# Kernel optimization log

Measured on AMD Instinct MI355X. Metric: run time of the kernel, lower is better.

Reference implementation:

```python
import jax, jax.numpy as jnp
import numpy as np

N_NODES = 100_000
E_OFF = 1_500_000
LATENT = 64
MP_STEPS = 3


def setup_inputs() -> dict:
    key = jax.random.key(0)
    ks = jax.random.split(key, 12)
    # lower-triangular graph: all self-loops + random off-diagonal edges with row >= col
    r = jax.random.randint(ks[0], (E_OFF,), 0, N_NODES)
    c = jax.random.randint(ks[1], (E_OFF,), 0, N_NODES)
    diag = jnp.arange(N_NODES)
    edge_row = jnp.concatenate([jnp.maximum(r, c), diag]).astype(jnp.int64)
    edge_col = jnp.concatenate([jnp.minimum(r, c), diag]).astype(jnp.int64)
    E = E_OFF + N_NODES
    # positive weights (gcn_norm takes deg^{-1/2} of weighted degree)
    edge_attr = jax.random.uniform(ks[2], (E,), jnp.float32) + 0.05
    x = jax.random.normal(ks[3], (N_NODES, 1), jnp.float32)
    L = LATENT
    def lin(k, fi, fo):
        return jax.random.normal(k, (fi, fo), jnp.float32) / np.sqrt(fi)
    return {
        "x": x,
        "edge_attr": edge_attr,
        "w_enc": lin(ks[4], 1, L), "b_enc": jnp.zeros((L,), jnp.float32),
        "conv1_w": jax.random.normal(ks[5], (MP_STEPS, L, L), jnp.float32) / np.sqrt(L),
        "conv1_b": jnp.zeros((MP_STEPS, L), jnp.float32),
        "conv2_w": jax.random.normal(ks[6], (MP_STEPS, L, L), jnp.float32) / np.sqrt(L),
        "conv2_b": jnp.zeros((MP_STEPS, L), jnp.float32),
        "dec_w1": lin(ks[7], 2 * L, L), "dec_b1": jnp.zeros((L,), jnp.float32),
        "dec_w2": lin(ks[8], L, 1), "dec_b2": jnp.zeros((1,), jnp.float32),
        "edge_row": edge_row,
        "edge_col": edge_col,
    }


def reference(x, edge_attr, w_enc, b_enc, conv1_w, conv1_b, conv2_w, conv2_b,
              dec_w1, dec_b1, dec_w2, dec_b2, edge_row, edge_col):
    N = x.shape[0]
    # GCN normalization (graph already contains all self-loops, so PyG's
    # add_remaining_self_loops is a no-op and keeps existing loop weights)
    deg = jax.ops.segment_sum(edge_attr, edge_col, num_segments=N)
    dinv = jnp.where(deg > 0, jax.lax.rsqrt(jnp.maximum(deg, 1e-30)), 0.0)
    norm = dinv[edge_row] * edge_attr * dinv[edge_col]  # [E]
    cnt = jnp.maximum(
        jax.ops.segment_sum(jnp.ones_like(edge_attr), edge_col, num_segments=N), 1.0
    )[:, None]  # mean aggregation denominator

    def gcn(h, W, b):
        m = (h @ W)[edge_row] * norm[:, None]           # [E, F] messages
        agg = jax.ops.segment_sum(m, edge_col, num_segments=N) / cnt
        return agg + b

    # node encoder: single Linear (no activation)
    h = x @ w_enc + b_enc
    for i in range(MP_STEPS):
        h = jax.nn.relu(gcn(h, conv1_w[i], conv1_b[i]))
        h = jax.nn.relu(gcn(h, conv2_w[i], conv2_b[i]))

    # edge decoder: gather endpoints, MLP [2L -> L -> 1]
    e = jnp.concatenate([h[edge_row], h[edge_col]], axis=1)
    e = jax.nn.relu(e @ dec_w1 + dec_b1)
    e = (e @ dec_w2 + dec_b2)[:, 0]                      # [E]
    vals = jnp.where(edge_row == edge_col, jax.nn.softplus(e), e)
    return vals
```

## Files before the change

kernel.cpp:

```cpp
#include <hip/hip_runtime.h>
#include <hip/hip_fp16.h>
#include <math.h>

#define L 64
#define FIXS 65536.0f
#define WAITCNT_LGKM0 0xC07F

#define FMAMIX_LO(acc, pkh, ws) \
    asm("v_fma_mix_f32 %0, %1, %2, %0 op_sel:[0,0,0] op_sel_hi:[1,0,0]" \
        : "+v"(acc) : "v"(pkh), "v"(ws))
#define FMAMIX_HI(acc, pkh, ws) \
    asm("v_fma_mix_f32 %0, %1, %2, %0 op_sel:[1,0,0] op_sel_hi:[1,0,0]" \
        : "+v"(acc) : "v"(pkh), "v"(ws))
#define PKADDRELU(d, a, b) \
    asm("v_pk_add_f16 %0, %1, %2\n\tv_pk_max_f16 %0, %0, 0" \
        : "=v"(d) : "v"(a), "v"(b))


__global__ void k_hist(const int* __restrict__ col, const float* __restrict__ attr,
                       unsigned* __restrict__ degcnt,
                       int* __restrict__ rank, int E) {
    int e = blockIdx.x * blockDim.x + threadIdx.x;
    if (e < E) {
        int c = col[e];
        unsigned fx = (unsigned)(int)rintf(attr[e] * FIXS);
        unsigned old = atomicAdd(&degcnt[c], (1u << 24) | fx);
        rank[e] = (int)(old >> 24);
    }
}

__global__ void k_dinv(const unsigned* __restrict__ degcnt,
                       float* __restrict__ dinv, int* __restrict__ cntI,
                       float* __restrict__ rcnt, int N) {
    int n = blockIdx.x * blockDim.x + threadIdx.x;
    if (n < N) {
        unsigned p = degcnt[n];
        unsigned cnt = p >> 24;
        float d = (float)(p & 0xFFFFFFu) * (1.0f / FIXS);
        dinv[n] = (d > 0.f) ? (1.0f / sqrtf(fmaxf(d, 1e-30f))) : 0.f;
        cntI[n] = (int)cnt;
        unsigned c = cnt ? cnt : 1u;
        rcnt[n] = 1.0f / (float)c;
    }
}


__global__ __launch_bounds__(256) void k_scan_a(const int* __restrict__ cntI,
                                                int* __restrict__ blockSums, int N) {
    __shared__ int red[4];
    int b = blockIdx.x, t = threadIdx.x;
    int base = b * 1024 + t * 4;
    int s = 0;
    #pragma unroll
    for (int i = 0; i < 4; ++i) { int idx = base + i; if (idx < N) s += cntI[idx]; }
    #pragma unroll
    for (int off = 32; off > 0; off >>= 1) s += __shfl_down(s, off);
    if ((t & 63) == 0) red[t >> 6] = s;
    __syncthreads();
    if (t == 0) blockSums[b] = red[0] + red[1] + red[2] + red[3];
}

__global__ __launch_bounds__(1024) void k_scan_b(int* __restrict__ blockSums, int B,
                                                 int* __restrict__ ptr, int N) {
    __shared__ int sh[1024];
    int t = threadIdx.x;
    sh[t] = (t < B) ? blockSums[t] : 0;
    __syncthreads();
    for (int off = 1; off < 1024; off <<= 1) {
        int v = (t >= off) ? sh[t - off] : 0;
        __syncthreads();
        sh[t] += v;
        __syncthreads();
    }
    if (t < B) blockSums[t] = (t == 0) ? 0 : sh[t - 1];
    if (t == B - 1) ptr[N] = sh[t];
}

__global__ __launch_bounds__(256) void k_scan_c(const int* __restrict__ cntI,
                                                const int* __restrict__ blockSums,
                                                int* __restrict__ ptr, int N) {
    __shared__ int th[256];
    int b = blockIdx.x, t = threadIdx.x;
    int base = b * 1024 + t * 4;
    int v[4]; int s = 0;
    #pragma unroll
    for (int i = 0; i < 4; ++i) {
        int idx = base + i;
        v[i] = (idx < N) ? cntI[idx] : 0;
        s += v[i];
    }
    th[t] = s;
    __syncthreads();
    for (int off = 1; off < 256; off <<= 1) {
        int x = (t >= off) ? th[t - off] : 0;
        __syncthreads();
        th[t] += x;
        __syncthreads();
    }
    int pre = ((t == 0) ? 0 : th[t - 1]) + blockSums[b];
    #pragma unroll
    for (int i = 0; i < 4; ++i) {
        int idx = base + i;
        if (idx < N) ptr[idx] = pre;
        pre += v[i];
    }
}

__global__ void k_scatter(const int* __restrict__ row, const int* __restrict__ col,
                          const float* __restrict__ attr, const float* __restrict__ dinv,
                          const int* __restrict__ colptr,
                          int* __restrict__ rank ,
                          unsigned* __restrict__ csrX, int E) {
    int e = blockIdx.x * blockDim.x + threadIdx.x;
    if (e < E) {
        int r = row[e], c = col[e];
        int pos = colptr[c] + rank[e];
        float nrm = dinv[r] * attr[e] * dinv[c];
        unsigned short nb = __half_as_ushort(__float2half(nrm));
        csrX[pos] = (unsigned)r | ((unsigned)nb << 17);
        rank[e] = pos;
    }
}


__global__ void k_encode(const float* __restrict__ x, const float* __restrict__ w_enc,
                         const float* __restrict__ b_enc, __half* __restrict__ h, int N) {
    int idx = blockIdx.x * blockDim.x + threadIdx.x;
    if (idx < N * L) {
        int n = idx >> 6, f = idx & 63;
        h[idx] = __float2half(x[n] * w_enc[f] + b_enc[f]);
    }
}


__global__ __launch_bounds__(256) void k_gcn(const uint2* __restrict__ h_in2,
        __half* __restrict__ h_out,
        const float* __restrict__ W, const float* __restrict__ bias,
        const int* __restrict__ colptr, const unsigned* __restrict__ csrX,
        const float* __restrict__ rcnt, int N) {
    __shared__ float sm[4][72];
    int lane = threadIdx.x & 63;
    int warp = threadIdx.x >> 6;
    int grp  = lane >> 4;
    int sub  = lane & 15;
    int wid  = (blockIdx.x * blockDim.x + threadIdx.x) >> 6;
    int nw   = (gridDim.x * blockDim.x) >> 6;
    float* smw = &sm[warp][0];

    float Wc[L];
    #pragma unroll
    for (int f = 0; f < L; ++f) Wc[f] = W[f * L + lane];
    float bl = bias[lane];

    int beg = 0, end = 0; unsigned mw = 0;
    if (wid < N) {
        beg = colptr[wid];
        end = colptr[wid + 1];
        if (beg + lane < end) mw = csrX[beg + lane];
    }

    for (int n = wid; n < N; n += nw) {
        int n2 = n + nw;
        int beg2 = 0, end2 = 0;
        if (n2 < N) { beg2 = colptr[n2]; end2 = colptr[n2 + 1]; }

        float sA0=0.f,sA1=0.f,sA2=0.f,sA3=0.f, sB0=0.f,sB1=0.f,sB2=0.f,sB3=0.f;
        float sC0=0.f,sC1=0.f,sC2=0.f,sC3=0.f, sD0=0.f,sD1=0.f,sD2=0.f,sD3=0.f;

        auto PROC = [&](unsigned mwv, int mm) {
            int kmax = (mm + 3) >> 2;
            int k = 0;
            for (; k + 4 <= kmax; k += 4) {
                int j0 = 4 * k + grp;
                unsigned x0 = (unsigned)__shfl((int)mwv, j0);
                unsigned x1 = (unsigned)__shfl((int)mwv, j0 + 4);
                unsigned x2 = (unsigned)__shfl((int)mwv, j0 + 8);
                unsigned x3 = (unsigned)__shfl((int)mwv, j0 + 12);
                int r0 = (int)(x0 & 0x1FFFFu), r1 = (int)(x1 & 0x1FFFFu);
                int r2 = (int)(x2 & 0x1FFFFu), r3 = (int)(x3 & 0x1FFFFu);
                float w0 = __half2float(__ushort_as_half((unsigned short)(x0 >> 17)));
                float w1 = __half2float(__ushort_as_half((unsigned short)(x1 >> 17)));
                float w2 = __half2float(__ushort_as_half((unsigned short)(x2 >> 17)));
                float w3 = __half2float(__ushort_as_half((unsigned short)(x3 >> 17)));
                uint2 q0 = h_in2[(size_t)r0 * 16 + sub];
                uint2 q1 = h_in2[(size_t)r1 * 16 + sub];
                uint2 q2 = h_in2[(size_t)r2 * 16 + sub];
                uint2 q3 = h_in2[(size_t)r3 * 16 + sub];
                FMAMIX_LO(sA0, q0.x, w0); FMAMIX_HI(sA1, q0.x, w0);
                FMAMIX_LO(sA2, q0.y, w0); FMAMIX_HI(sA3, q0.y, w0);
                FMAMIX_LO(sB0, q1.x, w1); FMAMIX_HI(sB1, q1.x, w1);
                FMAMIX_LO(sB2, q1.y, w1); FMAMIX_HI(sB3, q1.y, w1);
                FMAMIX_LO(sC0, q2.x, w2); FMAMIX_HI(sC1, q2.x, w2);
                FMAMIX_LO(sC2, q2.y, w2); FMAMIX_HI(sC3, q2.y, w2);
                FMAMIX_LO(sD0, q3.x, w3); FMAMIX_HI(sD1, q3.x, w3);
                FMAMIX_LO(sD2, q3.y, w3); FMAMIX_HI(sD3, q3.y, w3);
            }
            for (; k < kmax; ++k) {
                int j0 = 4 * k + grp;
                unsigned x0 = (unsigned)__shfl((int)mwv, j0);
                int   r0 = (int)(x0 & 0x1FFFFu);
                float w0 = __half2float(__ushort_as_half((unsigned short)(x0 >> 17)));
                uint2 q0 = h_in2[(size_t)r0 * 16 + sub];
                FMAMIX_LO(sA0, q0.x, w0); FMAMIX_HI(sA1, q0.x, w0);
                FMAMIX_LO(sA2, q0.y, w0); FMAMIX_HI(sA3, q0.y, w0);
            }
        };

        int m = end - beg; if (m > 64) m = 64;
        PROC(mw, m);
        for (int base = beg + 64; base < end; base += 64) {
            int mm = end - base; if (mm > 64) mm = 64;
            unsigned mwc = 0;
            if (lane < mm) mwc = csrX[base + lane];
            PROC(mwc, mm);
        }

        unsigned mw2 = 0;
        if (n2 < N && beg2 + lane < end2) mw2 = csrX[beg2 + lane];

        float sx = (sA0 + sB0) + (sC0 + sD0);
        float sy = (sA1 + sB1) + (sC1 + sD1);
        float sz = (sA2 + sB2) + (sC2 + sD2);
        float sw = (sA3 + sB3) + (sC3 + sD3);
        sx += __shfl_xor(sx, 16); sx += __shfl_xor(sx, 32);
        sy += __shfl_xor(sy, 16); sy += __shfl_xor(sy, 32);
        sz += __shfl_xor(sz, 16); sz += __shfl_xor(sz, 32);
        sw += __shfl_xor(sw, 16); sw += __shfl_xor(sw, 32);
        if (grp == 0) {
            smw[4 * sub + 0] = sx; smw[4 * sub + 1] = sy;
            smw[4 * sub + 2] = sz; smw[4 * sub + 3] = sw;
        }
        __builtin_amdgcn_s_waitcnt(WAITCNT_LGKM0);
        float a0 = 0.f, a1 = 0.f, a2 = 0.f, a3 = 0.f;
        const float4* smv = (const float4*)smw;
        #pragma unroll
        for (int q = 0; q < 16; ++q) {
            float4 sv = smv[q];
            a0 += sv.x * Wc[4 * q + 0];
            a1 += sv.y * Wc[4 * q + 1];
            a2 += sv.z * Wc[4 * q + 2];
            a3 += sv.w * Wc[4 * q + 3];
        }
        float o = ((a0 + a1) + (a2 + a3)) * rcnt[n] + bl;
        h_out[(size_t)n * L + lane] = __float2half(fmaxf(o, 0.f));

        beg = beg2; end = end2; mw = mw2;
    }
}


__global__ __launch_bounds__(256) void k_mv2(const __half* __restrict__ h,
        const float* __restrict__ W1, const float* __restrict__ b1,
        __half* __restrict__ U, __half* __restrict__ V, int N) {
    __shared__ float sm[4][72];
    int lane = threadIdx.x & 63;
    int warp = threadIdx.x >> 6;
    int wid  = (blockIdx.x * blockDim.x + threadIdx.x) >> 6;
    int nw   = (gridDim.x * blockDim.x) >> 6;
    float* smw = &sm[warp][0];
    float Wu[L], Wv[L];
    #pragma unroll
    for (int f = 0; f < L; ++f) Wu[f] = W1[f * L + lane];
    #pragma unroll
    for (int f = 0; f < L; ++f) Wv[f] = W1[(L + f) * L + lane];
    float bl = b1[lane];
    for (int n = wid; n < N; n += nw) {
        float hl = __half2float(h[(size_t)n * L + lane]);
        smw[lane] = hl;
        __builtin_amdgcn_s_waitcnt(WAITCNT_LGKM0);
        float a0 = 0.f, a1 = 0.f, c0 = 0.f, c1 = 0.f;
        const float4* smv = (const float4*)smw;
        #pragma unroll
        for (int q = 0; q < 16; ++q) {
            float4 sv = smv[q];
            a0 += sv.x * Wu[4 * q + 0] ; a1 += sv.y * Wu[4 * q + 1];
            a0 += sv.z * Wu[4 * q + 2] ; a1 += sv.w * Wu[4 * q + 3];
            c0 += sv.x * Wv[4 * q + 0] ; c1 += sv.y * Wv[4 * q + 1];
            c0 += sv.z * Wv[4 * q + 2] ; c1 += sv.w * Wv[4 * q + 3];
        }
        U[(size_t)n * L + lane] = __float2half((a0 + a1) + bl);
        V[(size_t)n * L + lane] = __float2half(c0 + c1);
        __builtin_amdgcn_s_waitcnt(WAITCNT_LGKM0);
    }
}


__global__ __launch_bounds__(256) void k_edge(const __half* __restrict__ U,
        const __half* __restrict__ V, const float* __restrict__ w2,
        const float* __restrict__ b2,
        const int* __restrict__ colptr, const unsigned* __restrict__ csrX,
        float* __restrict__ tmp, int N) {
    int lane = threadIdx.x & 63;
    int hf   = lane & 1;
    int wid  = (blockIdx.x * blockDim.x + threadIdx.x) >> 6;
    int nw   = (gridDim.x * blockDim.x) >> 6;
    float w2f[32];
    #pragma unroll
    for (int k = 0; k < 32; ++k) w2f[k] = w2[32 * hf + k];
    float b2v = b2[0];

    int beg = 0, end = 0; unsigned md0 = 0;
    if (wid < N) {
        beg = colptr[wid]; end = colptr[wid + 1];
        int ep = beg + (lane >> 1);
        if (ep < end) md0 = csrX[ep];
    }

    for (int n = wid; n < N; n += nw) {
        int n2 = n + nw;
        int beg2 = 0, end2 = 0;
        if (n2 < N) { beg2 = colptr[n2]; end2 = colptr[n2 + 1]; }

        const uint4* vrow = (const uint4*)(V + (size_t)n * L + 32 * hf);
        uint4 v0 = vrow[0], v1 = vrow[1], v2 = vrow[2], v3 = vrow[3];
        unsigned md = md0;
        for (int base = beg; base < end; base += 32) {
            int epos = base + (lane >> 1);
            if (epos < end) {
                int r = (int)(md & 0x1FFFFu);
                const uint4* urow = (const uint4*)(U + (size_t)r * L + 32 * hf);
                uint4 u0 = urow[0], u1 = urow[1], u2 = urow[2], u3 = urow[3];
                float p0 = 0.f, p1 = 0.f, p2 = 0.f, p3 = 0.f;
                #define DOT2X(uw, vw, B, pa, pb) { unsigned t_; \
                    PKADDRELU(t_, (uw), (vw)); \
                    FMAMIX_LO(pa, t_, w2f[B]); FMAMIX_HI(pb, t_, w2f[(B) + 1]); }
                DOT2X(u0.x, v0.x,  0, p0, p1) DOT2X(u0.y, v0.y,  2, p2, p3)
                DOT2X(u0.z, v0.z,  4, p0, p1) DOT2X(u0.w, v0.w,  6, p2, p3)
                DOT2X(u1.x, v1.x,  8, p0, p1) DOT2X(u1.y, v1.y, 10, p2, p3)
                DOT2X(u1.z, v1.z, 12, p0, p1) DOT2X(u1.w, v1.w, 14, p2, p3)
                DOT2X(u2.x, v2.x, 16, p0, p1) DOT2X(u2.y, v2.y, 18, p2, p3)
                DOT2X(u2.z, v2.z, 20, p0, p1) DOT2X(u2.w, v2.w, 22, p2, p3)
                DOT2X(u3.x, v3.x, 24, p0, p1) DOT2X(u3.y, v3.y, 26, p2, p3)
                DOT2X(u3.z, v3.z, 28, p0, p1) DOT2X(u3.w, v3.w, 30, p2, p3)
                #undef DOT2X
                float p = (p0 + p2) + (p1 + p3);
                p += __shfl_xor(p, 1);
                if (hf == 0) {
                    float val = p + b2v;
                    if (r == n) val = fmaxf(val, 0.f) + log1pf(expf(-fabsf(val)));
                    tmp[epos] = val;
                }
            }
            if (base + 32 < end) {
                int ep2 = base + 32 + (lane >> 1);
                md = (ep2 < end) ? csrX[ep2] : 0;
            }
        }

        unsigned mdn = 0;
        if (n2 < N) {
            int ep = beg2 + (lane >> 1);
            if (ep < end2) mdn = csrX[ep];
        }
        beg = beg2; end = end2; md0 = mdn;
    }
}


__global__ void k_perm(const int* __restrict__ epos, const float* __restrict__ tmp,
                       float* __restrict__ out, int E) {
    int e = blockIdx.x * blockDim.x + threadIdx.x;
    if (e < E) out[e] = tmp[epos[e]];
}


extern "C" void kernel_launch(void* const* d_in, const int* in_sizes, int n_in,
                              void* d_out, int out_size, void* d_ws, size_t ws_size,
                              hipStream_t stream) {
    const float* x     = (const float*)d_in[0];
    const float* attr  = (const float*)d_in[1];
    const float* w_enc = (const float*)d_in[2];
    const float* b_enc = (const float*)d_in[3];
    const float* c1w   = (const float*)d_in[4];
    const float* c1b   = (const float*)d_in[5];
    const float* c2w   = (const float*)d_in[6];
    const float* c2b   = (const float*)d_in[7];
    const float* dw1   = (const float*)d_in[8];
    const float* db1   = (const float*)d_in[9];
    const float* dw2   = (const float*)d_in[10];
    const float* db2   = (const float*)d_in[11];
    const int*   erow  = (const int*)d_in[12];
    const int*   ecol  = (const int*)d_in[13];
    int N = in_sizes[0];
    int E = in_sizes[1];
    float* out = (float*)d_out;

    char* w = (char*)d_ws;
    auto alloc = [&](size_t bytes) {
        char* p = w; w += (bytes + 255) & ~(size_t)255; return p;
    };
    unsigned* degcnt = (unsigned*)alloc((size_t)N * 4);
    size_t zbytes = (size_t)(w - (char*)d_ws);
    float* dinv   = (float*)alloc((size_t)N * 4);
    int*   cntI   = (int*)  alloc((size_t)N * 4);
    float* rcnt   = (float*)alloc((size_t)N * 4);
    int*   colptr = (int*)  alloc((size_t)(N + 1) * 4);
    int*   bsums  = (int*)  alloc(((size_t)(N + 1023) / 1024 + 1) * 4);
    int*   rank   = (int*)  alloc((size_t)E * 4);
    unsigned* csrX = (unsigned*)alloc((size_t)E * 4);
    float* tmp    = (float*)alloc((size_t)E * 4);
    __half* hA    = (__half*)alloc((size_t)N * L * 2);
    __half* hB    = (__half*)alloc((size_t)N * L * 2);
    __half* hU    = (__half*)alloc((size_t)N * L * 2);
    __half* hV    = (__half*)alloc((size_t)N * L * 2);
    (void)ws_size; (void)n_in; (void)out_size;

    (void)hipMemsetAsync(d_ws, 0, zbytes, stream);

    int eb = (E + 255) / 256;
    int nb = (N + 255) / 256;
    int B  = (N + 1023) / 1024;
    k_hist<<<eb, 256, 0, stream>>>(ecol, attr, degcnt, rank, E);
    k_dinv<<<nb, 256, 0, stream>>>(degcnt, dinv, cntI, rcnt, N);
    k_scan_a<<<B, 256, 0, stream>>>(cntI, bsums, N);
    k_scan_b<<<1, 1024, 0, stream>>>(bsums, B, colptr, N);
    k_scan_c<<<B, 256, 0, stream>>>(cntI, bsums, colptr, N);
    k_scatter<<<eb, 256, 0, stream>>>(erow, ecol, attr, dinv, colptr, rank, csrX, E);
    k_encode<<<(N * L + 255) / 256, 256, 0, stream>>>(x, w_enc, b_enc, hA, N);

    __half* hin = hA; __half* hout = hB;
    for (int i = 0; i < 3; ++i) {
        k_gcn<<<2048, 256, 0, stream>>>((const uint2*)hin, hout, c1w + i * L * L,
                                        c1b + i * L, colptr, csrX, rcnt, N);
        __half* t = hin; hin = hout; hout = t;
        k_gcn<<<2048, 256, 0, stream>>>((const uint2*)hin, hout, c2w + i * L * L,
                                        c2b + i * L, colptr, csrX, rcnt, N);
        t = hin; hin = hout; hout = t;
    }
    k_mv2<<<2048, 256, 0, stream>>>(hin, dw1, db1, hU, hV, N);
    k_edge<<<2048, 256, 0, stream>>>(hU, hV, dw2, db2, colptr, csrX, tmp, N);
    k_perm<<<eb, 256, 0, stream>>>(rank, tmp, out, E);
}
```

Before: 649.6 us.

## Use 16-byte row gathers with 8 edges per wave step in GCN aggregation

The GCN gather now has 8 lanes read one 128-byte fp16 row as uint4 loads, so each wave processes 8 edges at once instead of 4 with uint2 loads. Accumulation moves to two 8-wide accumulator arrays, remainder handling is unrolled, the reduction changes to three xor-shuffles, and rcnt is loaded earlier. Launch bounds hints are added to k_gcn and k_mv2, which may limit registers and cause spills given the 64-float weight column held per thread.

```diff
diff --git a/kernel.cpp b/kernel.cpp
--- a/kernel.cpp
+++ b/kernel.cpp
@@ -15,6 +15,16 @@
 #define PKADDRELU(d, a, b) \
     asm("v_pk_add_f16 %0, %1, %2\n\tv_pk_max_f16 %0, %0, 0" \
         : "=v"(d) : "v"(a), "v"(b))
+
+#define GLOAD(xw_, qv_, J) \
+    xw_ = (unsigned)__shfl((int)mwv, (J) * 8 + grp); \
+    qv_ = h4[(size_t)(xw_ & 0x1FFFFu) * 8 + sub];
+#define FMA8(A, qv_, xw_) { \
+    float wv_ = __half2float(__ushort_as_half((unsigned short)((xw_) >> 17))); \
+    FMAMIX_LO(A[0], (qv_).x, wv_); FMAMIX_HI(A[1], (qv_).x, wv_); \
+    FMAMIX_LO(A[2], (qv_).y, wv_); FMAMIX_HI(A[3], (qv_).y, wv_); \
+    FMAMIX_LO(A[4], (qv_).z, wv_); FMAMIX_HI(A[5], (qv_).z, wv_); \
+    FMAMIX_LO(A[6], (qv_).w, wv_); FMAMIX_HI(A[7], (qv_).w, wv_); }
 
 
 __global__ void k_hist(const int* __restrict__ col, const float* __restrict__ attr,
@@ -92,9 +102,9 @@
     th[t] = s;
     __syncthreads();
     for (int off = 1; off < 256; off <<= 1) {
-        int x = (t >= off) ? th[t - off] : 0;
+        int xv = (t >= off) ? th[t - off] : 0;
         __syncthreads();
-        th[t] += x;
+        th[t] += xv;
         __syncthreads();
     }
     int pre = ((t == 0) ? 0 : th[t - 1]) + blockSums[b];
@@ -133,7 +143,7 @@
 }
 
 
-__global__ __launch_bounds__(256) void k_gcn(const uint2* __restrict__ h_in2,
+__global__ __launch_bounds__(256, 4) void k_gcn(const uint4* __restrict__ h4,
         __half* __restrict__ h_out,
         const float* __restrict__ W, const float* __restrict__ bias,
         const int* __restrict__ colptr, const unsigned* __restrict__ csrX,
@@ -141,8 +151,8 @@
     __shared__ float sm[4][72];
     int lane = threadIdx.x & 63;
     int warp = threadIdx.x >> 6;
-    int grp  = lane >> 4;
-    int sub  = lane & 15;
+    int grp  = lane >> 3;
+    int sub  = lane & 7;
     int wid  = (blockIdx.x * blockDim.x + threadIdx.x) >> 6;
     int nw   = (gridDim.x * blockDim.x) >> 6;
     float* smw = &sm[warp][0];
@@ -163,46 +173,40 @@
         int n2 = n + nw;
         int beg2 = 0, end2 = 0;
         if (n2 < N) { beg2 = colptr[n2]; end2 = colptr[n2 + 1]; }
-
-        float sA0=0.f,sA1=0.f,sA2=0.f,sA3=0.f, sB0=0.f,sB1=0.f,sB2=0.f,sB3=0.f;
-        float sC0=0.f,sC1=0.f,sC2=0.f,sC3=0.f, sD0=0.f,sD1=0.f,sD2=0.f,sD3=0.f;
+        float rcv = rcnt[n];
+
+        float va[8], vb[8];
+        #pragma unroll
+        for (int i = 0; i < 8; ++i) { va[i] = 0.f; vb[i] = 0.f; }
 
         auto PROC = [&](unsigned mwv, int mm) {
-            int kmax = (mm + 3) >> 2;
+            int kmax = (mm + 7) >> 3;
             int k = 0;
-            for (; k + 4 <= kmax; k += 4) {
-                int j0 = 4 * k + grp;
-                unsigned x0 = (unsigned)__shfl((int)mwv, j0);
-                unsigned x1 = (unsigned)__shfl((int)mwv, j0 + 4);
-                unsigned x2 = (unsigned)__shfl((int)mwv, j0 + 8);
-                unsigned x3 = (unsigned)__shfl((int)mwv, j0 + 12);
-                int r0 = (int)(x0 & 0x1FFFFu), r1 = (int)(x1 & 0x1FFFFu);
-                int r2 = (int)(x2 & 0x1FFFFu), r3 = (int)(x3 & 0x1FFFFu);
-                float w0 = __half2float(__ushort_as_half((unsigned short)(x0 >> 17)));
-                float w1 = __half2float(__ushort_as_half((unsigned short)(x1 >> 17)));
-                float w2 = __half2float(__ushort_as_half((unsigned short)(x2 >> 17)));
-                float w3 = __half2float(__ushort_as_half((unsigned short)(x3 >> 17)));
-                uint2 q0 = h_in2[(size_t)r0 * 16 + sub];
-                uint2 q1 = h_in2[(size_t)r1 * 16 + sub];
-                uint2 q2 = h_in2[(size_t)r2 * 16 + sub];
-                uint2 q3 = h_in2[(size_t)r3 * 16 + sub];
-                FMAMIX_LO(sA0, q0.x, w0); FMAMIX_HI(sA1, q0.x, w0);
-                FMAMIX_LO(sA2, q0.y, w0); FMAMIX_HI(sA3, q0.y, w0);
-                FMAMIX_LO(sB0, q1.x, w1); FMAMIX_HI(sB1, q1.x, w1);
-                FMAMIX_LO(sB2, q1.y, w1); FMAMIX_HI(sB3, q1.y, w1);
-                FMAMIX_LO(sC0, q2.x, w2); FMAMIX_HI(sC1, q2.x, w2);
-                FMAMIX_LO(sC2, q2.y, w2); FMAMIX_HI(sC3, q2.y, w2);
-                FMAMIX_LO(sD0, q3.x, w3); FMAMIX_HI(sD1, q3.x, w3);
-                FMAMIX_LO(sD2, q3.y, w3); FMAMIX_HI(sD3, q3.y, w3);
-            }
-            for (; k < kmax; ++k) {
-                int j0 = 4 * k + grp;
-                unsigned x0 = (unsigned)__shfl((int)mwv, j0);
-                int   r0 = (int)(x0 & 0x1FFFFu);
-                float w0 = __half2float(__ushort_as_half((unsigned short)(x0 >> 17)));
-                uint2 q0 = h_in2[(size_t)r0 * 16 + sub];
-                FMAMIX_LO(sA0, q0.x, w0); FMAMIX_HI(sA1, q0.x, w0);
-                FMAMIX_LO(sA2, q0.y, w0); FMAMIX_HI(sA3, q0.y, w0);
+            while (k < kmax) {
+                int rem = kmax - k;
+                if (rem >= 4) {
+                    unsigned x0, x1, x2, x3; uint4 q0, q1, q2, q3;
+                    GLOAD(x0, q0, k) GLOAD(x1, q1, k + 1)
+                    GLOAD(x2, q2, k + 2) GLOAD(x3, q3, k + 3)
+                    FMA8(va, q0, x0) FMA8(vb, q1, x1)
+                    FMA8(va, q2, x2) FMA8(vb, q3, x3)
+                    k += 4;
+                } else if (rem == 3) {
+                    unsigned x0, x1, x2; uint4 q0, q1, q2;
+                    GLOAD(x0, q0, k) GLOAD(x1, q1, k + 1) GLOAD(x2, q2, k + 2)
+                    FMA8(va, q0, x0) FMA8(vb, q1, x1) FMA8(va, q2, x2)
+                    k += 3;
+                } else if (rem == 2) {
+                    unsigned x0, x1; uint4 q0, q1;
+                    GLOAD(x0, q0, k) GLOAD(x1, q1, k + 1)
+                    FMA8(va, q0, x0) FMA8(vb, q1, x1)
+                    k += 2;
+                } else {
+                    unsigned x0; uint4 q0;
+                    GLOAD(x0, q0, k)
+                    FMA8(va, q0, x0)
+                    k += 1;
+                }
             }
         };
 
@@ -218,17 +222,18 @@
         unsigned mw2 = 0;
         if (n2 < N && beg2 + lane < end2) mw2 = csrX[beg2 + lane];
 
-        float sx = (sA0 + sB0) + (sC0 + sD0);
-        float sy = (sA1 + sB1) + (sC1 + sD1);
-        float sz = (sA2 + sB2) + (sC2 + sD2);
-        float sw = (sA3 + sB3) + (sC3 + sD3);
-        sx += __shfl_xor(sx, 16); sx += __shfl_xor(sx, 32);
-        sy += __shfl_xor(sy, 16); sy += __shfl_xor(sy, 32);
-        sz += __shfl_xor(sz, 16); sz += __shfl_xor(sz, 32);
-        sw += __shfl_xor(sw, 16); sw += __shfl_xor(sw, 32);
-        if (grp == 0) {
-            smw[4 * sub + 0] = sx; smw[4 * sub + 1] = sy;
-            smw[4 * sub + 2] = sz; smw[4 * sub + 3] = sw;
+        float s[8];
+        #pragma unroll
+        for (int i = 0; i < 8; ++i) {
+            float v = va[i] + vb[i];
+            v += __shfl_xor(v, 8);
+            v += __shfl_xor(v, 16);
+            v += __shfl_xor(v, 32);
+            s[i] = v;
+        }
+        if (lane < 8) {
+            #pragma unroll
+            for (int i = 0; i < 8; ++i) smw[8 * lane + i] = s[i];
         }
         __builtin_amdgcn_s_waitcnt(WAITCNT_LGKM0);
         float a0 = 0.f, a1 = 0.f, a2 = 0.f, a3 = 0.f;
@@ -241,7 +246,7 @@
             a2 += sv.z * Wc[4 * q + 2];
             a3 += sv.w * Wc[4 * q + 3];
         }
-        float o = ((a0 + a1) + (a2 + a3)) * rcnt[n] + bl;
+        float o = ((a0 + a1) + (a2 + a3)) * rcv + bl;
         h_out[(size_t)n * L + lane] = __float2half(fmaxf(o, 0.f));
 
         beg = beg2; end = end2; mw = mw2;
@@ -249,7 +254,7 @@
 }
 
 
-__global__ __launch_bounds__(256) void k_mv2(const __half* __restrict__ h,
+__global__ __launch_bounds__(256, 2) void k_mv2(const __half* __restrict__ h,
         const float* __restrict__ W1, const float* __restrict__ b1,
         __half* __restrict__ U, __half* __restrict__ V, int N) {
     __shared__ float sm[4][72];
@@ -321,8 +326,8 @@
                 const uint4* urow = (const uint4*)(U + (size_t)r * L + 32 * hf);
                 uint4 u0 = urow[0], u1 = urow[1], u2 = urow[2], u3 = urow[3];
                 float p0 = 0.f, p1 = 0.f, p2 = 0.f, p3 = 0.f;
-                #define DOT2X(uw, vw, B, pa, pb) { unsigned t_; \
-                    PKADDRELU(t_, (uw), (vw)); \
+                #define DOT2X(uw_, vw_, B, pa, pb) { unsigned t_; \
+                    PKADDRELU(t_, (uw_), (vw_)); \
                     FMAMIX_LO(pa, t_, w2f[B]); FMAMIX_HI(pb, t_, w2f[(B) + 1]); }
                 DOT2X(u0.x, v0.x,  0, p0, p1) DOT2X(u0.y, v0.y,  2, p2, p3)
                 DOT2X(u0.z, v0.z,  4, p0, p1) DOT2X(u0.w, v0.w,  6, p2, p3)
@@ -420,10 +425,10 @@
 
     __half* hin = hA; __half* hout = hB;
     for (int i = 0; i < 3; ++i) {
-        k_gcn<<<2048, 256, 0, stream>>>((const uint2*)hin, hout, c1w + i * L * L,
+        k_gcn<<<2048, 256, 0, stream>>>((const uint4*)hin, hout, c1w + i * L * L,
                                         c1b + i * L, colptr, csrX, rcnt, N);
         __half* t = hin; hin = hout; hout = t;
-        k_gcn<<<2048, 256, 0, stream>>>((const uint2*)hin, hout, c2w + i * L * L,
+        k_gcn<<<2048, 256, 0, stream>>>((const uint4*)hin, hout, c2w + i * L * L,
                                         c2b + i * L, colptr, csrX, rcnt, N);
         t = hin; hin = hout; hout = t;
     }
```

Measured after the change: 648.1 us. No clear change (-0.2%).
